# Kernel tuning notes

Measured on AMD Instinct MI355X. Metric: run time of the kernel, lower is better.

The kernel has to match this reference:

```python
import jax, jax.numpy as jnp
import numpy as np


def _normalize_adj(edge_index, num_nodes):
    # add self loops
    loop = jnp.arange(num_nodes, dtype=edge_index.dtype)
    row = jnp.concatenate([edge_index[0], loop])
    col = jnp.concatenate([edge_index[1], loop])
    deg = jax.ops.segment_sum(jnp.ones(row.shape[0], jnp.float32), row,
                              num_segments=num_nodes)
    dis = jnp.where(deg > 0, jax.lax.rsqrt(deg), 0.0)  # deg^{-1/2}, inf->0
    ew = dis[row] * dis[col]
    return row, col, ew


def _gcn_conv(x, W, b, row, col, ew, num_nodes):
    h = x @ W.T + b                       # dense linear [N, out]
    msg = h[col] * ew[:, None]            # gather + scale [E', out]
    return jax.ops.segment_sum(msg, row, num_segments=num_nodes)  # scatter_add


def setup_inputs() -> dict:
    N, E, IN, HID, OUT = 100000, 1600000, 128, 128, 64
    key = jax.random.key(0)
    k1, k2, k3, k4 = jax.random.split(key, 4)
    x = jax.random.normal(k1, (N, IN), jnp.float32)
    edge_index = jax.random.randint(k2, (2, E), 0, N, jnp.int64)
    # xavier_uniform for weights, zero bias (as in reset_parameters)
    lim1 = float(np.sqrt(6.0 / (IN + HID)))
    lim2 = float(np.sqrt(6.0 / (HID + OUT)))
    W1 = jax.random.uniform(k3, (HID, IN), jnp.float32, -lim1, lim1)
    b1 = jnp.zeros((HID,), jnp.float32)
    W2 = jax.random.uniform(k4, (OUT, HID), jnp.float32, -lim2, lim2)
    b2 = jnp.zeros((OUT,), jnp.float32)
    return {"x": x, "edge_index": edge_index, "num_nodes": N,
            "W1": W1, "b1": b1, "W2": W2, "b2": b2}


def reference(x, edge_index, num_nodes, W1, b1, W2, b2):
    row, col, ew = _normalize_adj(edge_index, num_nodes)
    h = _gcn_conv(x, W1, b1, row, col, ew, num_nodes)
    h = jax.nn.relu(h)  # dropout is identity in eval mode
    out = _gcn_conv(h, W2, b2, row, col, ew, num_nodes)
    return out
```

## Files before the change

kernel.cpp:

```cpp
#include <hip/hip_runtime.h>
#include <hip/hip_bf16.h>
#include <stdint.h>


#define TPB 256
#define NBLK_C 256
#define TPB_C 1024
#define MAX_NB 2048

typedef __attribute__((ext_vector_type(8))) __bf16 bf16x8;
typedef __attribute__((ext_vector_type(4))) float f32x4;

__device__ __forceinline__ float bf16lo(unsigned u) { return __uint_as_float(u << 16); }
__device__ __forceinline__ float bf16hi(unsigned u) { return __uint_as_float(u & 0xffff0000u); }
__device__ __forceinline__ unsigned short f2bf(float f) {
    unsigned u = __float_as_uint(f);
    return (unsigned short)((u + 0x7fff + ((u >> 16) & 1)) >> 16);
}

__global__ void detect64_kernel(const int* __restrict__ ei32, int* __restrict__ flag) {
    if (threadIdx.x == 0 && blockIdx.x == 0) {
        int is64 = 1;
        for (int t = 0; t < 64; ++t) {
            if (ei32[2 * t + 1] != 0) { is64 = 0; break; }
        }
        *flag = is64;
    }
}

__global__ __launch_bounds__(TPB_C) void hist_extract_kernel(const void* __restrict__ ei, int E,
                                                             int CH,
                                                             const int* __restrict__ flag,
                                                             int* __restrict__ row32,
                                                             int* __restrict__ col32,
                                                             int* __restrict__ hist,
                                                             int NB, int N) {
    __shared__ int h[MAX_NB];
    int tid = threadIdx.x;
    for (int bin = tid; bin < NB; bin += TPB_C) h[bin] = 0;
    __syncthreads();

    int b = blockIdx.x;
    int s = b * CH;
    int end = min(E, s + CH);
    int is64 = *flag;
    unsigned uN = (unsigned)N;
    if (is64) {
        const long long* p = (const long long*)ei;
        for (int e = s + tid; e < end; e += TPB_C) {
            int r = (int)p[e];
            int c = (int)p[E + e];
            row32[e] = r;
            col32[e] = c;
            if ((unsigned)r < uN && (unsigned)c < uN) atomicAdd(&h[r >> 7], 1);
        }
    } else {
        const int* p = (const int*)ei;
        for (int e = s + tid; e < end; e += TPB_C) {
            int r = p[e];
            int c = p[E + e];
            row32[e] = r;
            col32[e] = c;
            if ((unsigned)r < uN && (unsigned)c < uN) atomicAdd(&h[r >> 7], 1);
        }
    }
    __syncthreads();
    for (int bin = tid; bin < NB; bin += TPB_C) hist[bin * NBLK_C + b] = h[bin];
}

__global__ __launch_bounds__(NBLK_C) void colscan_kernel(int* __restrict__ hist,
                                                         int* __restrict__ binTotal) {
    __shared__ int sm[NBLK_C];
    int bin = blockIdx.x;
    int tid = threadIdx.x;
    int v = hist[bin * NBLK_C + tid];
    sm[tid] = v;
    __syncthreads();
    for (int o = 1; o < NBLK_C; o <<= 1) {
        int x = (tid >= o) ? sm[tid - o] : 0;
        __syncthreads();
        sm[tid] += x;
        __syncthreads();
    }
    hist[bin * NBLK_C + tid] = sm[tid] - v;
    if (tid == NBLK_C - 1) binTotal[bin] = sm[NBLK_C - 1];
}

__global__ __launch_bounds__(1024) void binscan_kernel(const int* __restrict__ binTotal,
                                                       int* __restrict__ bucketStart, int NB) {
    __shared__ int sm[1024];
    int tid = threadIdx.x;
    int v = (tid < NB) ? binTotal[tid] : 0;
    sm[tid] = v;
    __syncthreads();
    for (int o = 1; o < 1024; o <<= 1) {
        int x = (tid >= o) ? sm[tid - o] : 0;
        __syncthreads();
        sm[tid] += x;
        __syncthreads();
    }
    if (tid < NB) bucketStart[tid] = sm[tid] - v;
}

__global__ __launch_bounds__(TPB_C) void scatter_kernel(const int* __restrict__ row32,
                                                        const int* __restrict__ col32, int E,
                                                        int CH,
                                                        const int* __restrict__ hist,
                                                        const int* __restrict__ bucketStart,
                                                        int* __restrict__ bucketed,
                                                        int NB, int N) {
    __shared__ int cur[MAX_NB];
    int tid = threadIdx.x;
    int b = blockIdx.x;
    for (int bin = tid; bin < NB; bin += TPB_C)
        cur[bin] = bucketStart[bin] + hist[bin * NBLK_C + b];
    __syncthreads();

    int s = b * CH;
    int end = min(E, s + CH);
    unsigned uN = (unsigned)N;
    for (int e = s + tid; e < end; e += TPB_C) {
        int r = row32[e];
        int c = col32[e];
        if ((unsigned)r < uN && (unsigned)c < uN) {
            int pos = atomicAdd(&cur[r >> 7], 1);
            bucketed[pos] = (c << 7) | (r & 127);
        }
    }
}

__global__ __launch_bounds__(TPB) void finecsr_kernel(const int* __restrict__ bucketed,
                                                      const int* __restrict__ bucketStart,
                                                      const int* __restrict__ binTotal,
                                                      int* __restrict__ offs,
                                                      int* __restrict__ cnt,
                                                      float* __restrict__ dis,
                                                      int* __restrict__ csr, int N) {
    __shared__ int c128[128];
    __shared__ int cur128[128];
    __shared__ int sm[TPB];
    int bin = blockIdx.x;
    int tid = threadIdx.x;
    int s = bucketStart[bin];
    int m = binTotal[bin];

    if (tid < 128) c128[tid] = 0;
    __syncthreads();
    for (int i = tid; i < m; i += TPB) atomicAdd(&c128[bucketed[s + i] & 127], 1);
    __syncthreads();

    int v = (tid < 128) ? c128[tid] : 0;
    sm[tid] = v;
    __syncthreads();
    for (int o = 1; o < 128; o <<= 1) {
        int x = (tid >= o) ? sm[tid - o] : 0;
        __syncthreads();
        sm[tid] += x;
        __syncthreads();
    }
    if (tid < 128) {
        int excl = sm[tid] - v;
        int r = bin * 128 + tid;
        if (r < N) {
            offs[r] = s + excl;
            cnt[r] = v;
            dis[r] = rsqrtf((float)v + 1.0f);
        }
        cur128[tid] = s + excl;
    }
    __syncthreads();
    for (int i = tid; i < m; i += TPB) {
        int p = bucketed[s + i];
        int pos = atomicAdd(&cur128[p & 127], 1);
        csr[pos] = p >> 7;
    }
}

template <int BN, bool INB16>
__global__ __launch_bounds__(256, 2) void gemm_mfma_kernel(const void* __restrict__ Xp,
                                                           const float* __restrict__ W,
                                                           const float* __restrict__ bias,
                                                           const float* __restrict__ dis,
                                                           unsigned short* __restrict__ Hb,
                                                           int N) {
    constexpr int XST = 136;
    __shared__ unsigned short Xs[128 * XST];
    __shared__ unsigned short Ws[BN * XST];

    const int tid = threadIdx.x;
    const int r0 = blockIdx.x * 128;

    if (INB16) {
        const ushort4* Xv = (const ushort4*)Xp;
        for (int idx = tid; idx < 128 * 32; idx += 256) {
            int row = idx >> 5, q = idx & 31;
            int rg = r0 + row;
            if (rg >= N) rg = N - 1;
            *(ushort4*)&Xs[row * XST + q * 4] = Xv[(size_t)rg * 32 + q];
        }
    } else {
        const float4* Xv = (const float4*)Xp;
        for (int idx = tid; idx < 128 * 32; idx += 256) {
            int row = idx >> 5, q = idx & 31;
            int rg = r0 + row;
            if (rg >= N) rg = N - 1;
            float4 v = Xv[(size_t)rg * 32 + q];
            ushort4 s = make_ushort4(f2bf(v.x), f2bf(v.y), f2bf(v.z), f2bf(v.w));
            *(ushort4*)&Xs[row * XST + q * 4] = s;
        }
    }
    {
        const float4* Wv = (const float4*)W;
        for (int idx = tid; idx < BN * 32; idx += 256) {
            int n = idx >> 5, q = idx & 31;
            float4 v = Wv[n * 32 + q];
            ushort4 s = make_ushort4(f2bf(v.x), f2bf(v.y), f2bf(v.z), f2bf(v.w));
            *(ushort4*)&Ws[n * XST + q * 4] = s;
        }
    }
    __syncthreads();

    constexpr int RT = (BN == 128) ? 4 : 2;
    constexpr int CT = 4;
    const int wave = tid >> 6, lane = tid & 63;
    const int l15 = lane & 15, q8 = lane >> 4;
    const int row0 = (BN == 128) ? (wave & 1) * 64 : wave * 32;
    const int col0 = (BN == 128) ? (wave >> 1) * 64 : 0;

    f32x4 zero = {0.f, 0.f, 0.f, 0.f};
    f32x4 acc[RT][CT];
#pragma unroll
    for (int rt = 0; rt < RT; ++rt)
#pragma unroll
        for (int ct = 0; ct < CT; ++ct) acc[rt][ct] = zero;

#pragma unroll
    for (int ks = 0; ks < 4; ++ks) {
        int ko = ks * 32 + q8 * 8;
        bf16x8 a[RT], b[CT];
#pragma unroll
        for (int rt = 0; rt < RT; ++rt)
            a[rt] = *(const bf16x8*)&Xs[(row0 + rt * 16 + l15) * XST + ko];
#pragma unroll
        for (int ct = 0; ct < CT; ++ct)
            b[ct] = *(const bf16x8*)&Ws[(col0 + ct * 16 + l15) * XST + ko];
#pragma unroll
        for (int rt = 0; rt < RT; ++rt)
#pragma unroll
            for (int ct = 0; ct < CT; ++ct)
                acc[rt][ct] = __builtin_amdgcn_mfma_f32_16x16x32_bf16(
                    a[rt], b[ct], acc[rt][ct], 0, 0, 0);
    }

    float bv[CT];
#pragma unroll
    for (int ct = 0; ct < CT; ++ct) bv[ct] = bias[col0 + ct * 16 + l15];
#pragma unroll
    for (int rt = 0; rt < RT; ++rt)
#pragma unroll
        for (int r = 0; r < 4; ++r) {
            int row = r0 + row0 + rt * 16 + q8 * 4 + r;
            if (row < N) {
                float dn = dis[row];
#pragma unroll
                for (int ct = 0; ct < CT; ++ct)
                    Hb[(size_t)row * BN + col0 + ct * 16 + l15] =
                        f2bf((acc[rt][ct][r] + bv[ct]) * dn);
            }
        }
}

template <int F, bool RELU, bool OB16>
__global__ __launch_bounds__(TPB) void agg_kernel(const unsigned short* __restrict__ Hb,
                                                  const int* __restrict__ csr,
                                                  const int* __restrict__ offs,
                                                  const int* __restrict__ cnt,
                                                  const float* __restrict__ dis,
                                                  void* __restrict__ outp, int N) {
    int w = (blockIdx.x * TPB + threadIdx.x) >> 6;
    if (w >= N) return;
    int lane = threadIdx.x & 63;
    float di = dis[w];
    int s = offs[w];
    int d = cnt[w];

    const unsigned* Hu = (const unsigned*)Hb;
    float2 acc;
    if (F == 128) {
        unsigned u = Hu[w * 64 + lane];
        acc.x = bf16lo(u);
        acc.y = bf16hi(u);
    } else {
        acc.x = __uint_as_float(((unsigned)Hb[w * 64 + lane]) << 16);
        acc.y = 0.0f;
    }

    for (int base = 0; base < d; base += 64) {
        int rem = d - base;
        if (rem > 64) rem = 64;
        int cl = (lane < rem) ? csr[s + base + lane] : 0;

        int e = 0;
        for (; e + 8 <= rem; e += 8) {
            int c0 = __shfl(cl, e + 0);
            int c1 = __shfl(cl, e + 1);
            int c2 = __shfl(cl, e + 2);
            int c3 = __shfl(cl, e + 3);
            int c4 = __shfl(cl, e + 4);
            int c5 = __shfl(cl, e + 5);
            int c6 = __shfl(cl, e + 6);
            int c7 = __shfl(cl, e + 7);
            if (F == 128) {
                unsigned u0 = Hu[c0 * 64 + lane];
                unsigned u1 = Hu[c1 * 64 + lane];
                unsigned u2 = Hu[c2 * 64 + lane];
                unsigned u3 = Hu[c3 * 64 + lane];
                unsigned u4 = Hu[c4 * 64 + lane];
                unsigned u5 = Hu[c5 * 64 + lane];
                unsigned u6 = Hu[c6 * 64 + lane];
                unsigned u7 = Hu[c7 * 64 + lane];
                acc.x += ((bf16lo(u0) + bf16lo(u1)) + (bf16lo(u2) + bf16lo(u3))) +
                         ((bf16lo(u4) + bf16lo(u5)) + (bf16lo(u6) + bf16lo(u7)));
                acc.y += ((bf16hi(u0) + bf16hi(u1)) + (bf16hi(u2) + bf16hi(u3))) +
                         ((bf16hi(u4) + bf16hi(u5)) + (bf16hi(u6) + bf16hi(u7)));
            } else {
                float h0 = __uint_as_float(((unsigned)Hb[c0 * 64 + lane]) << 16);
                float h1 = __uint_as_float(((unsigned)Hb[c1 * 64 + lane]) << 16);
                float h2 = __uint_as_float(((unsigned)Hb[c2 * 64 + lane]) << 16);
                float h3 = __uint_as_float(((unsigned)Hb[c3 * 64 + lane]) << 16);
                float h4 = __uint_as_float(((unsigned)Hb[c4 * 64 + lane]) << 16);
                float h5 = __uint_as_float(((unsigned)Hb[c5 * 64 + lane]) << 16);
                float h6 = __uint_as_float(((unsigned)Hb[c6 * 64 + lane]) << 16);
                float h7 = __uint_as_float(((unsigned)Hb[c7 * 64 + lane]) << 16);
                acc.x += ((h0 + h1) + (h2 + h3)) + ((h4 + h5) + (h6 + h7));
            }
        }
        for (; e < rem; ++e) {
            int c0 = __shfl(cl, e);
            if (F == 128) {
                unsigned u0 = Hu[c0 * 64 + lane];
                acc.x += bf16lo(u0);
                acc.y += bf16hi(u0);
            } else {
                acc.x += __uint_as_float(((unsigned)Hb[c0 * 64 + lane]) << 16);
            }
        }
    }

    acc.x *= di;
    acc.y *= di;
    if (RELU) { acc.x = fmaxf(acc.x, 0.f); acc.y = fmaxf(acc.y, 0.f); }
    if (OB16) {
        unsigned lo = f2bf(acc.x), hi = f2bf(acc.y);
        ((unsigned*)outp)[w * 64 + lane] = lo | (hi << 16);
    } else if (F == 128) {
        ((float2*)outp)[w * 64 + lane] = acc;
    } else {
        ((float*)outp)[w * 64 + lane] = acc.x;
    }
}

extern "C" void kernel_launch(void* const* d_in, const int* in_sizes, int n_in,
                              void* d_out, int out_size, void* d_ws, size_t ws_size,
                              hipStream_t stream) {
    const float* x  = (const float*)d_in[0];
    const void*  ei = d_in[1];
    const float* W1 = (const float*)d_in[3];
    const float* b1 = (const float*)d_in[4];
    const float* W2 = (const float*)d_in[5];
    const float* b2 = (const float*)d_in[6];
    float* out = (float*)d_out;

    const int IN = 128, HID = 128;
    const int N = in_sizes[0] / IN;
    const int E = in_sizes[1] / 2;
    const int NB = (N + 127) >> 7;
    const int CH = (E + NBLK_C - 1) / NBLK_C;

    char* ws = (char*)d_ws;
    size_t off = 0;
    auto alloc = [&](size_t bytes) -> void* {
        void* p = (void*)(ws + off);
        off += (bytes + 255) & ~(size_t)255;
        return p;
    };
    int*   flag     = (int*)alloc(256);
    int*   cnt      = (int*)alloc((size_t)N * 4);
    int*   offs     = (int*)alloc((size_t)N * 4);
    float* dis      = (float*)alloc((size_t)N * 4);
    int*   row32    = (int*)alloc((size_t)E * 4);
    int*   col32    = (int*)alloc((size_t)E * 4);
    int*   bucketed = (int*)alloc((size_t)E * 4);
    int*   csr      = (int*)alloc((size_t)E * 4);
    int*   hist     = (int*)alloc((size_t)NB * NBLK_C * 4);
    int*   binTotal = (int*)alloc((size_t)NB * 4);
    int*   bStart   = (int*)alloc((size_t)NB * 4);
    unsigned short* H1b = (unsigned short*)alloc((size_t)N * HID * 2);
    unsigned short* R1b = (unsigned short*)alloc((size_t)N * HID * 2);
    unsigned short* H2b = H1b;

    detect64_kernel<<<1, 64, 0, stream>>>((const int*)ei, flag);

    hist_extract_kernel<<<NBLK_C, TPB_C, 0, stream>>>(ei, E, CH, flag, row32, col32,
                                                      hist, NB, N);
    colscan_kernel<<<NB, NBLK_C, 0, stream>>>(hist, binTotal);
    binscan_kernel<<<1, 1024, 0, stream>>>(binTotal, bStart, NB);
    scatter_kernel<<<NBLK_C, TPB_C, 0, stream>>>(row32, col32, E, CH, hist, bStart,
                                                 bucketed, NB, N);
    finecsr_kernel<<<NB, TPB, 0, stream>>>(bucketed, bStart, binTotal,
                                           offs, cnt, dis, csr, N);

    int ngrid = (N + 127) / 128;

    gemm_mfma_kernel<128, false><<<ngrid, 256, 0, stream>>>(x, W1, b1, dis, H1b, N);
    agg_kernel<128, true, true><<<(N + 3) / 4, TPB, 0, stream>>>(H1b, csr, offs, cnt,
                                                                 dis, R1b, N);

    gemm_mfma_kernel<64, true><<<ngrid, 256, 0, stream>>>(R1b, W2, b2, dis, H2b, N);
    agg_kernel<64, false, false><<<(N + 3) / 4, TPB, 0, stream>>>(H2b, csr, offs, cnt,
                                                                  dis, out, N);
}
```

Before: 302.3 us.

## Gather four neighbors per wave with 16-lane groups and vector loads

The aggregation kernel now splits each 64-lane wave into four 16-lane groups. Each group gathers a different neighbor row with 8- or 16-byte vector loads, instead of every lane loading 2 or 4 bytes of the same row. Partial sums are combined across groups with xor shuffles, and 16 lanes write the output with vector stores. This is meant to raise memory-level parallelism and cut per-edge load instruction count, especially for the 64-feature layer. In exchange it adds masked loads for tail edges and a cross-lane reduction.

```diff
diff --git a/kernel.cpp b/kernel.cpp
--- a/kernel.cpp
+++ b/kernel.cpp
@@ -277,22 +277,38 @@
                                                   const int* __restrict__ cnt,
                                                   const float* __restrict__ dis,
                                                   void* __restrict__ outp, int N) {
+    constexpr int FPL = F / 16;
+    constexpr int NW = FPL / 2;
+    constexpr int RS = F / 2;
+
     int w = (blockIdx.x * TPB + threadIdx.x) >> 6;
     if (w >= N) return;
     int lane = threadIdx.x & 63;
+    int g = lane >> 4;
+    int fl = lane & 15;
+
     float di = dis[w];
     int s = offs[w];
     int d = cnt[w];
 
     const unsigned* Hu = (const unsigned*)Hb;
-    float2 acc;
-    if (F == 128) {
-        unsigned u = Hu[w * 64 + lane];
-        acc.x = bf16lo(u);
-        acc.y = bf16hi(u);
-    } else {
-        acc.x = __uint_as_float(((unsigned)Hb[w * 64 + lane]) << 16);
-        acc.y = 0.0f;
+
+    float acc[FPL];
+    {
+        unsigned su[NW];
+        if constexpr (NW == 4) {
+            uint4 v = *(const uint4*)&Hu[(size_t)w * RS + fl * NW];
+            su[0] = v.x; su[1] = v.y; su[2] = v.z; su[3] = v.w;
+        } else {
+            uint2 v = *(const uint2*)&Hu[(size_t)w * RS + fl * NW];
+            su[0] = v.x; su[1] = v.y;
+        }
+        float sm = (g == 0) ? 1.0f : 0.0f;
+#pragma unroll
+        for (int t = 0; t < NW; ++t) {
+            acc[2 * t] = sm * bf16lo(su[t]);
+            acc[2 * t + 1] = sm * bf16hi(su[t]);
+        }
     }
 
     for (int base = 0; base < d; base += 64) {
@@ -300,63 +316,68 @@
         if (rem > 64) rem = 64;
         int cl = (lane < rem) ? csr[s + base + lane] : 0;
 
-        int e = 0;
-        for (; e + 8 <= rem; e += 8) {
-            int c0 = __shfl(cl, e + 0);
-            int c1 = __shfl(cl, e + 1);
-            int c2 = __shfl(cl, e + 2);
-            int c3 = __shfl(cl, e + 3);
-            int c4 = __shfl(cl, e + 4);
-            int c5 = __shfl(cl, e + 5);
-            int c6 = __shfl(cl, e + 6);
-            int c7 = __shfl(cl, e + 7);
-            if (F == 128) {
-                unsigned u0 = Hu[c0 * 64 + lane];
-                unsigned u1 = Hu[c1 * 64 + lane];
-                unsigned u2 = Hu[c2 * 64 + lane];
-                unsigned u3 = Hu[c3 * 64 + lane];
-                unsigned u4 = Hu[c4 * 64 + lane];
-                unsigned u5 = Hu[c5 * 64 + lane];
-                unsigned u6 = Hu[c6 * 64 + lane];
-                unsigned u7 = Hu[c7 * 64 + lane];
-                acc.x += ((bf16lo(u0) + bf16lo(u1)) + (bf16lo(u2) + bf16lo(u3))) +
-                         ((bf16lo(u4) + bf16lo(u5)) + (bf16lo(u6) + bf16lo(u7)));
-                acc.y += ((bf16hi(u0) + bf16hi(u1)) + (bf16hi(u2) + bf16hi(u3))) +
-                         ((bf16hi(u4) + bf16hi(u5)) + (bf16hi(u6) + bf16hi(u7)));
+        for (int e = 0; e < rem; e += 16) {
+            int cc[4];
+            float m[4];
+#pragma unroll
+            for (int k = 0; k < 4; ++k) {
+                int idx = e + k * 4 + g;
+                cc[k] = __shfl(cl, idx & 63);
+                m[k] = (idx < rem) ? 1.0f : 0.0f;
+            }
+            unsigned u[4][NW];
+#pragma unroll
+            for (int k = 0; k < 4; ++k) {
+                if constexpr (NW == 4) {
+                    uint4 v = *(const uint4*)&Hu[(size_t)cc[k] * RS + fl * NW];
+                    u[k][0] = v.x; u[k][1] = v.y; u[k][2] = v.z; u[k][3] = v.w;
+                } else {
+                    uint2 v = *(const uint2*)&Hu[(size_t)cc[k] * RS + fl * NW];
+                    u[k][0] = v.x; u[k][1] = v.y;
+                }
+            }
+#pragma unroll
+            for (int k = 0; k < 4; ++k)
+#pragma unroll
+                for (int t = 0; t < NW; ++t) {
+                    acc[2 * t]     = fmaf(m[k], bf16lo(u[k][t]), acc[2 * t]);
+                    acc[2 * t + 1] = fmaf(m[k], bf16hi(u[k][t]), acc[2 * t + 1]);
+                }
+        }
+    }
+
+#pragma unroll
+    for (int off = 16; off < 64; off <<= 1)
+#pragma unroll
+        for (int j = 0; j < FPL; ++j) acc[j] += __shfl_xor(acc[j], off);
+
+#pragma unroll
+    for (int j = 0; j < FPL; ++j) {
+        acc[j] *= di;
+        if (RELU) acc[j] = fmaxf(acc[j], 0.0f);
+    }
+
+    if (lane < 16) {
+        if constexpr (OB16) {
+            unsigned dw[NW];
+#pragma unroll
+            for (int t = 0; t < NW; ++t)
+                dw[t] = (unsigned)f2bf(acc[2 * t]) | ((unsigned)f2bf(acc[2 * t + 1]) << 16);
+            unsigned* op = (unsigned*)outp;
+            if constexpr (NW == 4) {
+                *(uint4*)&op[(size_t)w * RS + fl * NW] = make_uint4(dw[0], dw[1], dw[2], dw[3]);
             } else {
-                float h0 = __uint_as_float(((unsigned)Hb[c0 * 64 + lane]) << 16);
-                float h1 = __uint_as_float(((unsigned)Hb[c1 * 64 + lane]) << 16);
-                float h2 = __uint_as_float(((unsigned)Hb[c2 * 64 + lane]) << 16);
-                float h3 = __uint_as_float(((unsigned)Hb[c3 * 64 + lane]) << 16);
-                float h4 = __uint_as_float(((unsigned)Hb[c4 * 64 + lane]) << 16);
-                float h5 = __uint_as_float(((unsigned)Hb[c5 * 64 + lane]) << 16);
-                float h6 = __uint_as_float(((unsigned)Hb[c6 * 64 + lane]) << 16);
-                float h7 = __uint_as_float(((unsigned)Hb[c7 * 64 + lane]) << 16);
-                acc.x += ((h0 + h1) + (h2 + h3)) + ((h4 + h5) + (h6 + h7));
+                *(uint2*)&op[(size_t)w * RS + fl * NW] = make_uint2(dw[0], dw[1]);
             }
-        }
-        for (; e < rem; ++e) {
-            int c0 = __shfl(cl, e);
-            if (F == 128) {
-                unsigned u0 = Hu[c0 * 64 + lane];
-                acc.x += bf16lo(u0);
-                acc.y += bf16hi(u0);
+        } else {
+            float4* op = (float4*)outp;
+            if constexpr (FPL == 4) {
+                op[(size_t)w * 16 + fl] = make_float4(acc[0], acc[1], acc[2], acc[3]);
             } else {
-                acc.x += __uint_as_float(((unsigned)Hb[c0 * 64 + lane]) << 16);
+                op[(size_t)w * 32 + fl * 2]     = make_float4(acc[0], acc[1], acc[2], acc[3]);
+                op[(size_t)w * 32 + fl * 2 + 1] = make_float4(acc[4], acc[5], acc[6], acc[7]);
             }
         }
-    }
-
-    acc.x *= di;
-    acc.y *= di;
-    if (RELU) { acc.x = fmaxf(acc.x, 0.f); acc.y = fmaxf(acc.y, 0.f); }
-    if (OB16) {
-        unsigned lo = f2bf(acc.x), hi = f2bf(acc.y);
-        ((unsigned*)outp)[w * 64 + lane] = lo | (hi << 16);
-    } else if (F == 128) {
-        ((float2*)outp)[w * 64 + lane] = acc;
-    } else {
-        ((float*)outp)[w * 64 + lane] = acc.x;
     }
 }
 
```

After: 282.8 us. 1.07x faster.
